# Performance work log

Measured on AMD Instinct MI355X. Metric: run time of the kernel, lower is better.

Reference implementation:

```python
import jax, jax.numpy as jnp
from jax import lax
import numpy as np

H = 128; L = 4; N_TOTAL = 4096; M = 4; S = 16384; K = 12; SK = S * K
MAX_DIST = 32; B = 64; NH = 4; DH = H // NH; BN_EPS = 1e-5


def _bn(x, g, b):
    # training-mode BatchNorm1d over rows (biased variance)
    mu = x.mean(0)
    var = x.var(0)
    return (x - mu) * lax.rsqrt(var + BN_EPS) * g + b


def _gine(x, src, dst, ea, eps, We, bWe, W1, b1, W2, b2):
    # PyG GINEConv: mlp((1+eps)*x + sum_j relu(x_j + lin(e_ji)))
    msg = jax.nn.relu(x[src] + ea @ We.T + bWe)
    agg = jax.ops.segment_sum(msg, dst, num_segments=x.shape[0])
    h = (1.0 + eps) * x + agg
    return jax.nn.relu(h @ W1.T + b1) @ W2.T + b2


def _forward(log_probs, atom_tab, bond_tab, dist_tab, logp_W, logp_b, lw, lb,
             bn_g, bn_b, eps, mha_in_W, mha_in_b, mha_out_W, mha_out_b, ro_g, ro_b,
             atom_ids, node_ids, intra_ei, intra_bond_ids, edge_index, canon_bond_ids, batch):
    sub_batch = jnp.arange(SK, dtype=jnp.int32) // K
    root_flat = jnp.arange(S, dtype=jnp.int32) * K
    valid_f = (node_ids >= 0).astype(jnp.float32)[:, None]
    clamped = jnp.maximum(node_ids, 0)
    x_flat = atom_tab[atom_ids][clamped]            # [SK, H]
    ea_flat = bond_tab[intra_bond_ids]              # [E_intra, H]
    edge_attr = bond_tab[canon_bond_ids]            # [E_canon, H]
    src, dst = intra_ei[0], intra_ei[1]

    # BFS distances from subgraph roots (min-plus relaxation, MAX_DIST sweeps)
    d0 = jnp.full((SK,), MAX_DIST, jnp.int32).at[root_flat].set(0)
    dist = lax.fori_loop(0, MAX_DIST, lambda i, d: d.at[dst].min(d[src] + 1), d0)
    dist = jnp.minimum(dist, MAX_DIST)
    dist_pe = dist_tab[dist]

    logp_pe = jax.nn.relu(log_probs[sub_batch][:, None] @ logp_W.T + logp_b)
    h = (x_flat + dist_pe + logp_pe) * valid_f

    is_root_f = jnp.zeros((SK, 1), jnp.float32).at[root_flat].set(1.0)
    root_ids = node_ids[root_flat]                  # canonical id of each root (>=0)
    cnt = jnp.maximum(jax.ops.segment_sum(jnp.ones((S,), jnp.float32), root_ids,
                                          num_segments=N_TOTAL), 1.0)

    for l in range(L):
        W = lw[l]; bv = lb[l]
        h1 = _gine(h, src, dst, ea_flat, eps[l, 0], W[0], bv[0], W[1], bv[1], W[2], bv[2])
        h1 = _bn(h1, bn_g[l, 0], bn_b[l, 0]) * valid_f
        h_root_b = h[sub_batch * K]
        h_nr = h @ W[3].T + bv[3] + h_root_b @ W[4].T + bv[4]
        h_can = jax.ops.segment_sum(h[root_flat], root_ids, num_segments=N_TOTAL) / cnt[:, None]
        h_int = _gine(h_can, edge_index[0], edge_index[1], edge_attr, eps[l, 1],
                      W[5], bv[5], W[6], bv[6], W[7], bv[7])
        h_int = _bn(h_int, bn_g[l, 1], bn_b[l, 1])
        h_ib = h_int[clamped] * valid_f
        out = is_root_f * (h1 + h_ib) + (1.0 - is_root_f) * (h1 + h_nr)
        h = jax.nn.relu(out) * valid_f

    # subgraph sum-pool (invalid rows are zeroed so scatter of zeros is a no-op)
    h_sub = jax.ops.segment_sum(h * valid_f, sub_batch, num_segments=S)
    order = jnp.argsort(root_ids)                   # stable by default
    h2 = h_sub[order].reshape(N_TOTAL, M, H)

    # MultiheadAttention over the m subgraphs of each canonical node
    qkv = h2 @ mha_in_W.T + mha_in_b
    q, k_, v = jnp.split(qkv, 3, axis=-1)
    hd = lambda t: t.reshape(N_TOTAL, M, NH, DH).transpose(0, 2, 1, 3)
    q, k_, v = hd(q), hd(k_), hd(v)
    scale = np.float32(1.0 / np.sqrt(DH))
    attn = jax.nn.softmax(jnp.einsum('nhqd,nhkd->nhqk', q, k_) * scale, axis=-1)
    o = jnp.einsum('nhqk,nhkd->nhqd', attn, v).transpose(0, 2, 1, 3).reshape(N_TOTAL, M, H)
    h_attn = o @ mha_out_W.T + mha_out_b + h2
    node_emb = _bn(h_attn.mean(1), ro_g, ro_b)
    return jax.ops.segment_sum(node_emb, batch, num_segments=B)


def setup_inputs() -> dict:
    key = jax.random.key(0)
    ks = jax.random.split(key, 32)
    rn = lambda i, sh, sc=0.1: (jax.random.normal(ks[i], sh) * sc).astype(jnp.float32)
    atom_ids = jax.random.randint(ks[0], (N_TOTAL,), 0, 64, dtype=jnp.int32)
    nid = jax.random.randint(ks[1], (S, K), 0, N_TOTAL, dtype=jnp.int32)
    pad = jax.random.uniform(ks[2], (S, K)) < 0.1
    nid = jnp.where(pad, -1, nid)
    nid = nid.at[:, 0].set(jnp.arange(S, dtype=jnp.int32) // M)  # roots: each canonical node m times
    node_ids = nid.reshape(-1)
    flat = jnp.arange(SK, dtype=jnp.int32).reshape(S, K)
    intra_ei = jnp.stack([flat[:, :-1].reshape(-1), flat[:, 1:].reshape(-1)])  # chains per subgraph
    intra_bond_ids = jax.random.randint(ks[3], (S * (K - 1),), 0, 8, dtype=jnp.int32)
    edge_index = jax.random.randint(ks[4], (2, N_TOTAL * 8), 0, N_TOTAL, dtype=jnp.int32)
    canon_bond_ids = jax.random.randint(ks[5], (N_TOTAL * 8,), 0, 8, dtype=jnp.int32)
    batch = jnp.arange(N_TOTAL, dtype=jnp.int32) // (N_TOTAL // B)
    log_probs = jax.random.normal(ks[6], (S,), dtype=jnp.float32)
    return dict(
        atom_ids=atom_ids, node_ids=node_ids, intra_ei=intra_ei,
        intra_bond_ids=intra_bond_ids, edge_index=edge_index,
        canon_bond_ids=canon_bond_ids, batch=batch, log_probs=log_probs,
        atom_tab=rn(7, (64, H)), bond_tab=rn(8, (8, H)), dist_tab=rn(9, (MAX_DIST + 1, H)),
        logp_W=rn(10, (H, 1)), logp_b=jnp.zeros((H,), jnp.float32),
        lw=rn(11, (L, 8, H, H)), lb=jnp.zeros((L, 8, H), jnp.float32),
        bn_g=jnp.ones((L, 2, H), jnp.float32), bn_b=jnp.zeros((L, 2, H), jnp.float32),
        eps=jnp.zeros((L, 2), jnp.float32),
        mha_in_W=rn(12, (3 * H, H)), mha_in_b=jnp.zeros((3 * H,), jnp.float32),
        mha_out_W=rn(13, (H, H)), mha_out_b=jnp.zeros((H,), jnp.float32),
        ro_g=jnp.ones((H,), jnp.float32), ro_b=jnp.zeros((H,), jnp.float32))


def reference(atom_ids, node_ids, intra_ei, intra_bond_ids, edge_index, canon_bond_ids,
              batch, log_probs, atom_tab, bond_tab, dist_tab, logp_W, logp_b, lw, lb,
              bn_g, bn_b, eps, mha_in_W, mha_in_b, mha_out_W, mha_out_b, ro_g, ro_b):
    return _forward(log_probs, atom_tab, bond_tab, dist_tab, logp_W, logp_b, lw, lb,
                    bn_g, bn_b, eps, mha_in_W, mha_in_b, mha_out_W, mha_out_b, ro_g, ro_b,
                    atom_ids, node_ids, intra_ei, intra_bond_ids, edge_index, canon_bond_ids, batch)
```

## Files before the change

### kernel.cpp

```cpp
#include <hip/hip_runtime.h>
#include <math.h>

#define DEV static __device__ __forceinline__

constexpr int H    = 128;
constexpr int Ksub = 12;
constexpr int S    = 16384;
constexpr int SK   = S * Ksub;
constexpr int NTOT = 4096;

DEV float4 ld4(const float* p) { return *(const float4*)p; }
DEV void   st4(float* p, float4 v) { *(float4*)p = v; }
DEV float4 add4(float4 a, float4 b) { return make_float4(a.x+b.x, a.y+b.y, a.z+b.z, a.w+b.w); }
DEV float4 relu4(float4 a) { return make_float4(fmaxf(a.x,0.f), fmaxf(a.y,0.f), fmaxf(a.z,0.f), fmaxf(a.w,0.f)); }

template<int PRO, int EPI>
__global__ __launch_bounds__(256, 4) void mm128(
    const float* __restrict__ X, const float* __restrict__ Wm,
    const float* __restrict__ bias, float* __restrict__ Y,
    const float* __restrict__ eps_p,
    const float* __restrict__ a1, const float* __restrict__ a2,
    const float* __restrict__ a3, const int* __restrict__ ids,
    float* __restrict__ stats, const float* __restrict__ bng,
    const float* __restrict__ bnb, float invR, size_t ybstride)
{
  __shared__ float smem[2 * 32 * 132];
  float (*Xs)[132] = (float(*)[132])smem;
  float (*Ws)[132] = (float(*)[132])(smem + 32 * 132);
  const int tid  = threadIdx.x;
  const int row0 = blockIdx.x * 128;
  const int yb   = blockIdx.y;
  Wm   += (size_t)yb * (H * H);
  bias += yb * H;
  Y    += (size_t)yb * ybstride;

  const int tc  = tid & 15;
  const int tr  = tid >> 4;
  const int kq4 = (tid & 7) * 4;
  const int rb  = tid >> 3;

  float scal = 1.0f;
  if (PRO == 1 || PRO == 3) scal = 1.0f + eps_p[0];

  float acc[8][8];
#pragma unroll
  for (int i = 0; i < 8; ++i)
#pragma unroll
    for (int j = 0; j < 8; ++j) acc[i][j] = 0.f;

  for (int kk = 0; kk < 128; kk += 32) {
    __syncthreads();
#pragma unroll
    for (int p = 0; p < 4; ++p) {
      int r = rb + 32 * p;
      int grow = row0 + r;
      float4 wv = ld4(Wm + (size_t)r * H + kk + kq4);
      float4 xv;
      if (PRO == 2) xv = ld4(X + ((size_t)grow * Ksub) * H + kk + kq4);
      else          xv = ld4(X + (size_t)grow * H + kk + kq4);
      if (PRO == 1) {
        float4 a = ld4(a1 + (size_t)grow * H + kk + kq4);
        xv.x = fmaf(scal, xv.x, a.x); xv.y = fmaf(scal, xv.y, a.y);
        xv.z = fmaf(scal, xv.z, a.z); xv.w = fmaf(scal, xv.w, a.w);
      }
      if (PRO == 3) {
        int q = grow % Ksub;
        float m0 = 0.f, m1 = 0.f, m2 = 0.f, m3 = 0.f;
        if (q) {
          int bid = ids[(grow / Ksub) * (Ksub - 1) + q - 1];
          float4 hp = ld4(X + (size_t)(grow - 1) * H + kk + kq4);
          float4 bp = ld4(a1 + (size_t)bid * H + kk + kq4);
          m0 = fmaxf(hp.x + bp.x, 0.f); m1 = fmaxf(hp.y + bp.y, 0.f);
          m2 = fmaxf(hp.z + bp.z, 0.f); m3 = fmaxf(hp.w + bp.w, 0.f);
        }
        xv.x = fmaf(scal, xv.x, m0); xv.y = fmaf(scal, xv.y, m1);
        xv.z = fmaf(scal, xv.z, m2); xv.w = fmaf(scal, xv.w, m3);
      }
      Xs[kq4 + 0][r] = xv.x; Xs[kq4 + 1][r] = xv.y;
      Xs[kq4 + 2][r] = xv.z; Xs[kq4 + 3][r] = xv.w;
      Ws[kq4 + 0][r] = wv.x; Ws[kq4 + 1][r] = wv.y;
      Ws[kq4 + 2][r] = wv.z; Ws[kq4 + 3][r] = wv.w;
    }
    __syncthreads();
#pragma unroll 4
    for (int k = 0; k < 32; ++k) {
      float xv[8], wv[8];
      *(float4*)&xv[0] = *(const float4*)&Xs[k][4 * tr];
      *(float4*)&xv[4] = *(const float4*)&Xs[k][64 + 4 * tr];
      *(float4*)&wv[0] = *(const float4*)&Ws[k][4 * tc];
      *(float4*)&wv[4] = *(const float4*)&Ws[k][64 + 4 * tc];
#pragma unroll
      for (int i = 0; i < 8; ++i)
#pragma unroll
        for (int j = 0; j < 8; ++j) acc[i][j] = fmaf(xv[i], wv[j], acc[i][j]);
    }
  }

  float4 bias0 = ld4(bias + 4 * tc);
  float4 bias1 = ld4(bias + 64 + 4 * tc);
  float4 mu0, mu1, rs0, rs1, g0, g1, bb0, bb1;
  if (EPI == 3) {
    float4 s0 = ld4(stats + 4 * tc),        s1 = ld4(stats + 64 + 4 * tc);
    float4 q0 = ld4(stats + 128 + 4 * tc),  q1 = ld4(stats + 128 + 64 + 4 * tc);
    mu0 = make_float4(s0.x * invR, s0.y * invR, s0.z * invR, s0.w * invR);
    mu1 = make_float4(s1.x * invR, s1.y * invR, s1.z * invR, s1.w * invR);
    rs0 = make_float4(rsqrtf(q0.x * invR - mu0.x * mu0.x + 1e-5f),
                      rsqrtf(q0.y * invR - mu0.y * mu0.y + 1e-5f),
                      rsqrtf(q0.z * invR - mu0.z * mu0.z + 1e-5f),
                      rsqrtf(q0.w * invR - mu0.w * mu0.w + 1e-5f));
    rs1 = make_float4(rsqrtf(q1.x * invR - mu1.x * mu1.x + 1e-5f),
                      rsqrtf(q1.y * invR - mu1.y * mu1.y + 1e-5f),
                      rsqrtf(q1.z * invR - mu1.z * mu1.z + 1e-5f),
                      rsqrtf(q1.w * invR - mu1.w * mu1.w + 1e-5f));
    g0 = ld4(bng + 4 * tc); g1 = ld4(bng + 64 + 4 * tc);
    bb0 = ld4(bnb + 4 * tc); bb1 = ld4(bnb + 64 + 4 * tc);
  }
  float ps[8], pq[8];
  if (EPI == 2) {
#pragma unroll
    for (int j = 0; j < 8; ++j) { ps[j] = 0.f; pq[j] = 0.f; }
  }

#pragma unroll
  for (int i = 0; i < 8; ++i) {
    int gr = row0 + ((i < 4) ? 4 * tr + i : 60 + 4 * tr + i);
    float4 y0 = make_float4(acc[i][0] + bias0.x, acc[i][1] + bias0.y,
                            acc[i][2] + bias0.z, acc[i][3] + bias0.w);
    float4 y1 = make_float4(acc[i][4] + bias1.x, acc[i][5] + bias1.y,
                            acc[i][6] + bias1.z, acc[i][7] + bias1.w);
    if (EPI == 1) { y0 = relu4(y0); y1 = relu4(y1); }
    if (EPI == 4) {
      y0 = add4(y0, ld4(a1 + (size_t)gr * H + 4 * tc));
      y1 = add4(y1, ld4(a1 + (size_t)gr * H + 64 + 4 * tc));
    }
    if (EPI == 3) {
      int nid = ids[gr];
      float vf = (nid >= 0) ? 1.f : 0.f;
      bool root = (gr % Ksub) == 0;
      float4 t0 = ld4(a1 + (size_t)gr * H + 4 * tc);
      float4 t1v = ld4(a1 + (size_t)gr * H + 64 + 4 * tc);
      float4 h10 = make_float4(fmaf((t0.x - mu0.x) * rs0.x, g0.x, bb0.x),
                               fmaf((t0.y - mu0.y) * rs0.y, g0.y, bb0.y),
                               fmaf((t0.z - mu0.z) * rs0.z, g0.z, bb0.z),
                               fmaf((t0.w - mu0.w) * rs0.w, g0.w, bb0.w));
      float4 h11 = make_float4(fmaf((t1v.x - mu1.x) * rs1.x, g1.x, bb1.x),
                               fmaf((t1v.y - mu1.y) * rs1.y, g1.y, bb1.y),
                               fmaf((t1v.z - mu1.z) * rs1.z, g1.z, bb1.z),
                               fmaf((t1v.w - mu1.w) * rs1.w, g1.w, bb1.w));
      float4 add0, add1;
      if (root) {
        add0 = ld4(a2 + (size_t)nid * H + 4 * tc);
        add1 = ld4(a2 + (size_t)nid * H + 64 + 4 * tc);
      } else {
        add0 = add4(y0, ld4(a3 + (size_t)(gr / Ksub) * H + 4 * tc));
        add1 = add4(y1, ld4(a3 + (size_t)(gr / Ksub) * H + 64 + 4 * tc));
      }
      y0 = make_float4(vf * fmaxf(h10.x + add0.x, 0.f), vf * fmaxf(h10.y + add0.y, 0.f),
                       vf * fmaxf(h10.z + add0.z, 0.f), vf * fmaxf(h10.w + add0.w, 0.f));
      y1 = make_float4(vf * fmaxf(h11.x + add1.x, 0.f), vf * fmaxf(h11.y + add1.y, 0.f),
                       vf * fmaxf(h11.z + add1.z, 0.f), vf * fmaxf(h11.w + add1.w, 0.f));
    }
    st4(Y + (size_t)gr * H + 4 * tc, y0);
    st4(Y + (size_t)gr * H + 64 + 4 * tc, y1);
    if (EPI == 2) {
      ps[0] += y0.x; pq[0] += y0.x * y0.x; ps[1] += y0.y; pq[1] += y0.y * y0.y;
      ps[2] += y0.z; pq[2] += y0.z * y0.z; ps[3] += y0.w; pq[3] += y0.w * y0.w;
      ps[4] += y1.x; pq[4] += y1.x * y1.x; ps[5] += y1.y; pq[5] += y1.y * y1.y;
      ps[6] += y1.z; pq[6] += y1.z * y1.z; ps[7] += y1.w; pq[7] += y1.w * y1.w;
    }
  }
  if (EPI == 2) {
    __syncthreads();
    float* redS = smem;
    float* redQ = smem + 2048;
#pragma unroll
    for (int j = 0; j < 8; ++j) {
      int c = (j < 4) ? 4 * tc + j : 60 + 4 * tc + j;
      redS[tr * 128 + c] = ps[j];
      redQ[tr * 128 + c] = pq[j];
    }
    __syncthreads();
    if (tid < 128) {
      float s = 0.f, q = 0.f;
#pragma unroll
      for (int t = 0; t < 16; ++t) { s += redS[t * 128 + tid]; q += redQ[t * 128 + tid]; }
      atomicAdd(stats + tid, s);
      atomicAdd(stats + 128 + tid, q);
    }
  }
}

__global__ void k_init_h(float* __restrict__ h, const int* __restrict__ node_ids,
                         const int* __restrict__ atom_ids,
                         const float* __restrict__ atom_tab, const float* __restrict__ dist_tab,
                         const float* __restrict__ log_probs, const float* __restrict__ logp_W,
                         const float* __restrict__ logp_b)
{
  int idx = blockIdx.x * 256 + threadIdx.x;
  if (idx >= SK * 32) return;
  int r = idx >> 5, c4 = (idx & 31) * 4;
  int nid = node_ids[r];
  float valid = nid >= 0 ? 1.f : 0.f;
  int cl = nid >= 0 ? nid : 0;
  int aid = atom_ids[cl];
  int dd = r % Ksub;
  float lp = log_probs[r / Ksub];
  float4 at = ld4(atom_tab + aid * H + c4);
  float4 dt = ld4(dist_tab + dd * H + c4);
  float4 w  = ld4(logp_W + c4);
  float4 bb = ld4(logp_b + c4);
  float4 o;
  o.x = (at.x + dt.x + fmaxf(fmaf(lp, w.x, bb.x), 0.f)) * valid;
  o.y = (at.y + dt.y + fmaxf(fmaf(lp, w.y, bb.y), 0.f)) * valid;
  o.z = (at.z + dt.z + fmaxf(fmaf(lp, w.z, bb.z), 0.f)) * valid;
  o.w = (at.w + dt.w + fmaxf(fmaf(lp, w.w, bb.w), 0.f)) * valid;
  st4(h + (size_t)r * H + c4, o);
}

__global__ void k_bond_all(const float* __restrict__ bt, const float* __restrict__ lw,
                           const float* __restrict__ lb, float* __restrict__ bp_all)
{
  int m = blockIdx.x;
  int c = threadIdx.x;
  int l = m >> 1, wsel = (m & 1) ? 5 : 0;
  const float* W = lw + ((size_t)l * 8 + wsel) * H * H;
  const float* b = lb + ((size_t)l * 8 + wsel) * H;
  for (int j = 0; j < 8; ++j) {
    float s = b[c];
    for (int k = 0; k < H; ++k) s = fmaf(bt[j * H + k], W[c * H + k], s);
    bp_all[(size_t)(m * 8 + j) * H + c] = s;
  }
}

__global__ void k_c1(const float* __restrict__ h, float* __restrict__ c1) {
  int idx = blockIdx.x * 256 + threadIdx.x;
  if (idx >= NTOT * 32) return;
  int n = idx >> 5, c4 = (idx & 31) * 4;
  float4 a = ld4(h + ((size_t)(4 * n + 0) * Ksub) * H + c4);
  float4 b = ld4(h + ((size_t)(4 * n + 1) * Ksub) * H + c4);
  float4 c = ld4(h + ((size_t)(4 * n + 2) * Ksub) * H + c4);
  float4 d = ld4(h + ((size_t)(4 * n + 3) * Ksub) * H + c4);
  float4 o;
  o.x = (a.x + b.x + c.x + d.x) * 0.25f;
  o.y = (a.y + b.y + c.y + d.y) * 0.25f;
  o.z = (a.z + b.z + c.z + d.z) * 0.25f;
  o.w = (a.w + b.w + c.w + d.w) * 0.25f;
  st4(c1 + (size_t)n * H + c4, o);
}

__global__ void k_agg(const float* __restrict__ x, const int* __restrict__ src,
                      const int* __restrict__ dst, const int* __restrict__ bid,
                      const float* __restrict__ bp, float* __restrict__ out, int E)
{
  int idx = blockIdx.x * 256 + threadIdx.x;
  if (idx >= E * 32) return;
  int e = idx >> 5, c4 = (idx & 31) * 4;
  int sv = src[e], dv = dst[e], bb = bid[e];
  float4 m = relu4(add4(ld4(x + (size_t)sv * H + c4), ld4(bp + (size_t)bb * H + c4)));
  float* o = out + (size_t)dv * H + c4;
  atomicAdd(o + 0, m.x); atomicAdd(o + 1, m.y);
  atomicAdd(o + 2, m.z); atomicAdd(o + 3, m.w);
}

__global__ __launch_bounds__(256) void k_bn_stats(const float* __restrict__ X, int R,
                                                  float* __restrict__ stats) {
  __shared__ float sh[2][256];
  int c = threadIdx.x & 127;
  int rr = threadIdx.x >> 7;
  float s = 0.f, s2 = 0.f;
  for (int r = blockIdx.x * 2 + rr; r < R; r += gridDim.x * 2) {
    float v = X[(size_t)r * H + c];
    s += v; s2 += v * v;
  }
  sh[0][threadIdx.x] = s; sh[1][threadIdx.x] = s2;
  __syncthreads();
  if (rr == 0) {
    atomicAdd(&stats[c],       s  + sh[0][threadIdx.x + 128]);
    atomicAdd(&stats[128 + c], s2 + sh[1][threadIdx.x + 128]);
  }
}

__global__ void k_bn_apply(float* __restrict__ X, int R, const float* __restrict__ stats,
                           const float* __restrict__ g, const float* __restrict__ b)
{
  int idx = blockIdx.x * 256 + threadIdx.x;
  if (idx >= R * 32) return;
  int r = idx >> 5, c4 = (idx & 31) * 4;
  float invR = 1.0f / (float)R;
  float4 sm = ld4(stats + c4);
  float4 sq = ld4(stats + 128 + c4);
  float4 gv = ld4(g + c4), bv = ld4(b + c4);
  float mu0 = sm.x * invR, mu1 = sm.y * invR, mu2 = sm.z * invR, mu3 = sm.w * invR;
  float k0 = rsqrtf(sq.x * invR - mu0 * mu0 + 1e-5f);
  float k1 = rsqrtf(sq.y * invR - mu1 * mu1 + 1e-5f);
  float k2 = rsqrtf(sq.z * invR - mu2 * mu2 + 1e-5f);
  float k3 = rsqrtf(sq.w * invR - mu3 * mu3 + 1e-5f);
  float4 x = ld4(X + (size_t)r * H + c4);
  float4 o;
  o.x = (x.x - mu0) * k0 * gv.x + bv.x;
  o.y = (x.y - mu1) * k1 * gv.y + bv.y;
  o.z = (x.z - mu2) * k2 * gv.z + bv.z;
  o.w = (x.w - mu3) * k3 * gv.w + bv.w;
  st4(X + (size_t)r * H + c4, o);
}

__global__ void k_pool(const float* __restrict__ h, float* __restrict__ hsub) {
  int idx = blockIdx.x * 256 + threadIdx.x;
  if (idx >= S * 32) return;
  int s = idx >> 5, c4 = (idx & 31) * 4;
  float4 acc = make_float4(0.f, 0.f, 0.f, 0.f);
  const float* p = h + ((size_t)s * Ksub) * H + c4;
#pragma unroll
  for (int j = 0; j < Ksub; ++j) acc = add4(acc, ld4(p + j * H));
  st4(hsub + (size_t)s * H + c4, acc);
}

__global__ __launch_bounds__(128) void k_attn(const float* __restrict__ qb,
                                              const float* __restrict__ kb,
                                              const float* __restrict__ vb,
                                              float* __restrict__ ob)
{
  int n = blockIdx.x;
  int c = threadIdx.x;
  float q[4], kv[4], vv[4];
#pragma unroll
  for (int m = 0; m < 4; ++m) {
    q[m]  = qb[(size_t)(n * 4 + m) * H + c];
    kv[m] = kb[(size_t)(n * 4 + m) * H + c];
    vv[m] = vb[(size_t)(n * 4 + m) * H + c];
  }
  const float scale = 0.17677669529663687f;
  float sc[4][4];
#pragma unroll
  for (int m1 = 0; m1 < 4; ++m1)
#pragma unroll
    for (int m2 = 0; m2 < 4; ++m2) {
      float p = q[m1] * kv[m2];
#pragma unroll
      for (int off = 16; off > 0; off >>= 1) p += __shfl_xor(p, off, 32);
      sc[m1][m2] = p * scale;
    }
#pragma unroll
  for (int m1 = 0; m1 < 4; ++m1) {
    float mx = fmaxf(fmaxf(sc[m1][0], sc[m1][1]), fmaxf(sc[m1][2], sc[m1][3]));
    float e0 = expf(sc[m1][0] - mx), e1 = expf(sc[m1][1] - mx);
    float e2 = expf(sc[m1][2] - mx), e3 = expf(sc[m1][3] - mx);
    float inv = 1.f / (e0 + e1 + e2 + e3);
    ob[(size_t)(n * 4 + m1) * H + c] =
        (e0 * vv[0] + e1 * vv[1] + e2 * vv[2] + e3 * vv[3]) * inv;
  }
}

__global__ void k_mean(const float* __restrict__ ha, float* __restrict__ ne) {
  int idx = blockIdx.x * 256 + threadIdx.x;
  if (idx >= NTOT * 32) return;
  int n = idx >> 5, c4 = (idx & 31) * 4;
  float4 a = ld4(ha + (size_t)(n * 4 + 0) * H + c4);
  float4 b = ld4(ha + (size_t)(n * 4 + 1) * H + c4);
  float4 c = ld4(ha + (size_t)(n * 4 + 2) * H + c4);
  float4 d = ld4(ha + (size_t)(n * 4 + 3) * H + c4);
  float4 o;
  o.x = (a.x + b.x + c.x + d.x) * 0.25f;
  o.y = (a.y + b.y + c.y + d.y) * 0.25f;
  o.z = (a.z + b.z + c.z + d.z) * 0.25f;
  o.w = (a.w + b.w + c.w + d.w) * 0.25f;
  st4(ne + (size_t)n * H + c4, o);
}

__global__ __launch_bounds__(128) void k_finalsum(const float* __restrict__ ne,
                                                  const float* __restrict__ stats,
                                                  const float* __restrict__ g,
                                                  const float* __restrict__ b,
                                                  float* __restrict__ out)
{
  int bg = blockIdx.x;
  int c = threadIdx.x;
  const float invR = 1.0f / (float)NTOT;
  float mu = stats[c] * invR;
  float rs = rsqrtf(stats[128 + c] * invR - mu * mu + 1e-5f);
  float gg = g[c], bb = b[c];
  float acc = 0.f;
  for (int r = 0; r < 64; ++r) {
    float v = ne[(size_t)(bg * 64 + r) * H + c];
    acc += (v - mu) * rs * gg + bb;
  }
  out[(size_t)bg * H + c] = acc;
}

extern "C" void kernel_launch(void* const* d_in, const int* in_sizes, int n_in,
                              void* d_out, int out_size, void* d_ws, size_t ws_size,
                              hipStream_t stream)
{
  const int*   atom_ids   = (const int*)d_in[0];
  const int*   node_ids   = (const int*)d_in[1];
  const int*   intra_bid  = (const int*)d_in[3];
  const int*   edge_index = (const int*)d_in[4];
  const int*   canon_bid  = (const int*)d_in[5];
  const float* log_probs  = (const float*)d_in[7];
  const float* atom_tab   = (const float*)d_in[8];
  const float* bond_tab   = (const float*)d_in[9];
  const float* dist_tab   = (const float*)d_in[10];
  const float* logp_W     = (const float*)d_in[11];
  const float* logp_b     = (const float*)d_in[12];
  const float* lw         = (const float*)d_in[13];
  const float* lb         = (const float*)d_in[14];
  const float* bn_g       = (const float*)d_in[15];
  const float* bn_b       = (const float*)d_in[16];
  const float* eps        = (const float*)d_in[17];
  const float* mha_in_W   = (const float*)d_in[18];
  const float* mha_in_b   = (const float*)d_in[19];
  const float* mha_out_W  = (const float*)d_in[20];
  const float* mha_out_b  = (const float*)d_in[21];
  const float* ro_g       = (const float*)d_in[22];
  const float* ro_b       = (const float*)d_in[23];

  const int E2 = in_sizes[4] / 2;
  const int* src2 = edge_index, *dst2 = edge_index + E2;

  float* ws = (float*)d_ws;
  const size_t SKH = (size_t)SK * H;
  float* h      = ws;
  float* t      = ws + SKH;
  float* rproj  = ws + 2 * SKH;
  float* c1     = rproj + (size_t)S * H;
  float* c2     = c1 + (size_t)NTOT * H;
  float* c3     = c2 + (size_t)NTOT * H;
  float* ne     = c3 + (size_t)NTOT * H;
  float* bp_all = ne + (size_t)NTOT * H;
  float* statsA = bp_all + 64 * H;
  float* hsub = t;
  float* qkv  = t + (size_t)S * H;
  float* ob   = qkv + 3 * (size_t)S * H;
  float* out  = (float*)d_out;

  hipMemsetAsync(statsA, 0, 9 * 256 * sizeof(float), stream);
  k_bond_all<<<8, 128, 0, stream>>>(bond_tab, lw, lb, bp_all);
  k_init_h<<<(SK * 32 + 255) / 256, 256, 0, stream>>>(h, node_ids, atom_ids,
      atom_tab, dist_tab, log_probs, logp_W, logp_b);

  for (int l = 0; l < 4; ++l) {
    const float* W  = lw + (size_t)l * 8 * H * H;
    const float* bb = lb + (size_t)l * 8 * H;
    const float* g0 = bn_g + (l * 2 + 0) * H, *b0  = bn_b + (l * 2 + 0) * H;
    const float* g1 = bn_g + (l * 2 + 1) * H, *b1v = bn_b + (l * 2 + 1) * H;
    const float* eps0 = eps + l * 2, *eps1 = eps + l * 2 + 1;
    float* st0 = statsA + (size_t)l * 512;
    float* st1 = statsA + (size_t)l * 512 + 256;
    const float* bp0 = bp_all + (size_t)(l * 2 + 0) * 8 * H;
    const float* bp1 = bp_all + (size_t)(l * 2 + 1) * 8 * H;

    mm128<3, 1><<<dim3(SK / 128, 1), 256, 0, stream>>>(h, W + 1 * H * H, bb + 1 * H, t,
        eps0, bp0, nullptr, nullptr, intra_bid, nullptr, nullptr, nullptr, 0.f, 0);
    mm128<0, 2><<<dim3(SK / 128, 1), 256, 0, stream>>>(t, W + 2 * H * H, bb + 2 * H, t,
        nullptr, nullptr, nullptr, nullptr, nullptr, st0, nullptr, nullptr, 0.f, 0);
    mm128<2, 0><<<dim3(S / 128, 1), 256, 0, stream>>>(h, W + 4 * H * H, bb + 4 * H, rproj,
        nullptr, nullptr, nullptr, nullptr, nullptr, nullptr, nullptr, nullptr, 0.f, 0);
    k_c1<<<(NTOT * 32 + 255) / 256, 256, 0, stream>>>(h, c1);
    hipMemsetAsync(c2, 0, (size_t)NTOT * H * sizeof(float), stream);
    k_agg<<<(E2 * 32 + 255) / 256, 256, 0, stream>>>(c1, src2, dst2, canon_bid, bp1, c2, E2);
    mm128<1, 1><<<dim3(NTOT / 128, 1), 256, 0, stream>>>(c1, W + 6 * H * H, bb + 6 * H, c2,
        eps1, c2, nullptr, nullptr, nullptr, nullptr, nullptr, nullptr, 0.f, 0);
    mm128<0, 2><<<dim3(NTOT / 128, 1), 256, 0, stream>>>(c2, W + 7 * H * H, bb + 7 * H, c3,
        nullptr, nullptr, nullptr, nullptr, nullptr, st1, nullptr, nullptr, 0.f, 0);
    k_bn_apply<<<(NTOT * 32 + 255) / 256, 256, 0, stream>>>(c3, NTOT, st1, g1, b1v);
    mm128<0, 3><<<dim3(SK / 128, 1), 256, 0, stream>>>(h, W + 3 * H * H, bb + 3 * H, h,
        nullptr, t, c3, rproj, node_ids, st0, g0, b0, 1.0f / (float)SK, 0);
  }

  k_pool<<<(S * 32 + 255) / 256, 256, 0, stream>>>(h, hsub);
  mm128<0, 0><<<dim3(S / 128, 3), 256, 0, stream>>>(hsub, mha_in_W, mha_in_b, qkv,
      nullptr, nullptr, nullptr, nullptr, nullptr, nullptr, nullptr, nullptr, 0.f,
      (size_t)S * H);
  k_attn<<<NTOT, 128, 0, stream>>>(qkv, qkv + (size_t)S * H, qkv + 2 * (size_t)S * H, ob);
  mm128<0, 4><<<dim3(S / 128, 1), 256, 0, stream>>>(ob, mha_out_W, mha_out_b, ob,
      nullptr, hsub, nullptr, nullptr, nullptr, nullptr, nullptr, nullptr, 0.f, 0);
  k_mean<<<(NTOT * 32 + 255) / 256, 256, 0, stream>>>(ob, ne);
  float* stF = statsA + 8 * 256;
  k_bn_stats<<<512, 256, 0, stream>>>(ne, NTOT, stF);
  k_finalsum<<<64, 128, 0, stream>>>(ne, stF, ro_g, ro_b, out);
}
```

Before: 1.798 ms.

## Replace FP32 SIMT GEMMs with split-bf16 MFMA matrix-core kernels

Replaces the shared-memory FP32 FMA GEMM with a kernel that splits activations and weights into bf16 hi/lo pairs and runs three MFMA 16x16x32 products per tile, recovering near-FP32 accuracy on matrix cores. Weights are pre-split once per call by a new k_split kernel. The GIN node-level prologue (eps scaling plus aggregate) moves into a separate k_prep2 kernel, and the rproj GEMM is reordered. Operands now load directly from global memory without LDS staging, and the three-term split is slightly less exact than true FP32.

```diff
diff --git a/kernel.cpp b/kernel.cpp
--- a/kernel.cpp
+++ b/kernel.cpp
@@ -9,184 +9,187 @@
 constexpr int SK   = S * Ksub;
 constexpr int NTOT = 4096;
 
+typedef __attribute__((ext_vector_type(8))) short bhalf8;
+typedef __attribute__((ext_vector_type(4))) float floatx4;
+
 DEV float4 ld4(const float* p) { return *(const float4*)p; }
 DEV void   st4(float* p, float4 v) { *(float4*)p = v; }
-DEV float4 add4(float4 a, float4 b) { return make_float4(a.x+b.x, a.y+b.y, a.z+b.z, a.w+b.w); }
-DEV float4 relu4(float4 a) { return make_float4(fmaxf(a.x,0.f), fmaxf(a.y,0.f), fmaxf(a.z,0.f), fmaxf(a.w,0.f)); }
+
+DEV ushort f2b(float f) {
+  unsigned x = __float_as_uint(f);
+  return (ushort)((x + 0x7FFFu + ((x >> 16) & 1u)) >> 16);
+}
+DEV float b2f(ushort u) { return __uint_as_float(((unsigned)u) << 16); }
+
+DEV void split8(const float* v, bhalf8& hi, bhalf8& lo) {
+#pragma unroll
+  for (int j = 0; j < 8; ++j) {
+    ushort hv = f2b(v[j]);
+    hi[j] = (short)hv;
+    lo[j] = (short)f2b(v[j] - b2f(hv));
+  }
+}
 
 template<int PRO, int EPI>
-__global__ __launch_bounds__(256, 4) void mm128(
-    const float* __restrict__ X, const float* __restrict__ Wm,
-    const float* __restrict__ bias, float* __restrict__ Y,
-    const float* __restrict__ eps_p,
+__global__ __launch_bounds__(256) void mmB(
+    const float* __restrict__ X, const ushort* __restrict__ Whi,
+    const ushort* __restrict__ Wlo, const float* __restrict__ bias,
+    float* __restrict__ Y,
     const float* __restrict__ a1, const float* __restrict__ a2,
     const float* __restrict__ a3, const int* __restrict__ ids,
     float* __restrict__ stats, const float* __restrict__ bng,
-    const float* __restrict__ bnb, float invR, size_t ybstride)
-{
-  __shared__ float smem[2 * 32 * 132];
-  float (*Xs)[132] = (float(*)[132])smem;
-  float (*Ws)[132] = (float(*)[132])(smem + 32 * 132);
+    const float* __restrict__ bnb, const float* __restrict__ eps_p,
+    float invR, size_t ybstride)
+{
+  __shared__ float sred[2][8][128];
   const int tid  = threadIdx.x;
+  const int lane = tid & 63, wv = tid >> 6;
+  const int wr = (wv >> 1) * 64, wc = (wv & 1) * 64;
+  const int m = lane & 15, q = lane >> 4;
   const int row0 = blockIdx.x * 128;
-  const int yb   = blockIdx.y;
-  Wm   += (size_t)yb * (H * H);
+  const int yb = blockIdx.y;
+  Whi  += (size_t)yb * (H * H);
+  Wlo  += (size_t)yb * (H * H);
   bias += yb * H;
   Y    += (size_t)yb * ybstride;
 
-  const int tc  = tid & 15;
-  const int tr  = tid >> 4;
-  const int kq4 = (tid & 7) * 4;
-  const int rb  = tid >> 3;
-
   float scal = 1.0f;
-  if (PRO == 1 || PRO == 3) scal = 1.0f + eps_p[0];
-
-  float acc[8][8];
-#pragma unroll
-  for (int i = 0; i < 8; ++i)
-#pragma unroll
-    for (int j = 0; j < 8; ++j) acc[i][j] = 0.f;
-
-  for (int kk = 0; kk < 128; kk += 32) {
-    __syncthreads();
-#pragma unroll
-    for (int p = 0; p < 4; ++p) {
-      int r = rb + 32 * p;
-      int grow = row0 + r;
-      float4 wv = ld4(Wm + (size_t)r * H + kk + kq4);
-      float4 xv;
-      if (PRO == 2) xv = ld4(X + ((size_t)grow * Ksub) * H + kk + kq4);
-      else          xv = ld4(X + (size_t)grow * H + kk + kq4);
-      if (PRO == 1) {
-        float4 a = ld4(a1 + (size_t)grow * H + kk + kq4);
-        xv.x = fmaf(scal, xv.x, a.x); xv.y = fmaf(scal, xv.y, a.y);
-        xv.z = fmaf(scal, xv.z, a.z); xv.w = fmaf(scal, xv.w, a.w);
+  if (PRO == 3) scal = 1.0f + eps_p[0];
+
+  floatx4 acc[4][4];
+#pragma unroll
+  for (int i = 0; i < 4; ++i)
+#pragma unroll
+    for (int j = 0; j < 4; ++j) acc[i][j] = (floatx4){0.f, 0.f, 0.f, 0.f};
+
+  size_t arow[4], brow[4];
+  int qi[4];
+  const float* bprow[4];
+#pragma unroll
+  for (int i = 0; i < 4; ++i) {
+    int grow = row0 + wr + 16 * i + m;
+    arow[i] = (size_t)(PRO == 2 ? grow * Ksub : grow) * H;
+    brow[i] = (size_t)(wc + 16 * i + m) * H;
+    qi[i] = 0; bprow[i] = nullptr;
+    if (PRO == 3) {
+      qi[i] = grow % Ksub;
+      if (qi[i]) bprow[i] = a1 + (size_t)ids[(grow / Ksub) * (Ksub - 1) + qi[i] - 1] * H;
+    }
+  }
+
+#pragma unroll
+  for (int s = 0; s < 4; ++s) {
+    const int ko = s * 32 + q * 8;
+    bhalf8 bhi[4], blo[4];
+#pragma unroll
+    for (int j = 0; j < 4; ++j) {
+      bhi[j] = *(const bhalf8*)(Whi + brow[j] + ko);
+      blo[j] = *(const bhalf8*)(Wlo + brow[j] + ko);
+    }
+    bhalf8 ahi[4], alo[4];
+#pragma unroll
+    for (int i = 0; i < 4; ++i) {
+      float xv[8];
+      *(float4*)&xv[0] = ld4(X + arow[i] + ko);
+      *(float4*)&xv[4] = ld4(X + arow[i] + ko + 4);
+      if (PRO == 3) {
+        if (qi[i]) {
+          float pv[8], bv[8];
+          *(float4*)&pv[0] = ld4(X + arow[i] - H + ko);
+          *(float4*)&pv[4] = ld4(X + arow[i] - H + ko + 4);
+          *(float4*)&bv[0] = ld4(bprow[i] + ko);
+          *(float4*)&bv[4] = ld4(bprow[i] + ko + 4);
+#pragma unroll
+          for (int j = 0; j < 8; ++j)
+            xv[j] = fmaf(scal, xv[j], fmaxf(pv[j] + bv[j], 0.f));
+        } else {
+#pragma unroll
+          for (int j = 0; j < 8; ++j) xv[j] *= scal;
+        }
       }
-      if (PRO == 3) {
-        int q = grow % Ksub;
-        float m0 = 0.f, m1 = 0.f, m2 = 0.f, m3 = 0.f;
-        if (q) {
-          int bid = ids[(grow / Ksub) * (Ksub - 1) + q - 1];
-          float4 hp = ld4(X + (size_t)(grow - 1) * H + kk + kq4);
-          float4 bp = ld4(a1 + (size_t)bid * H + kk + kq4);
-          m0 = fmaxf(hp.x + bp.x, 0.f); m1 = fmaxf(hp.y + bp.y, 0.f);
-          m2 = fmaxf(hp.z + bp.z, 0.f); m3 = fmaxf(hp.w + bp.w, 0.f);
+      split8(xv, ahi[i], alo[i]);
+    }
+#pragma unroll
+    for (int i = 0; i < 4; ++i)
+#pragma unroll
+      for (int j = 0; j < 4; ++j) {
+        acc[i][j] = __builtin_amdgcn_mfma_f32_16x16x32_bf16(ahi[i], bhi[j], acc[i][j], 0, 0, 0);
+        acc[i][j] = __builtin_amdgcn_mfma_f32_16x16x32_bf16(ahi[i], blo[j], acc[i][j], 0, 0, 0);
+        acc[i][j] = __builtin_amdgcn_mfma_f32_16x16x32_bf16(alo[i], bhi[j], acc[i][j], 0, 0, 0);
+      }
+  }
+
+  __syncthreads();
+
+  float psum[4], psq[4];
+#pragma unroll
+  for (int j = 0; j < 4; ++j) { psum[j] = 0.f; psq[j] = 0.f; }
+
+#pragma unroll
+  for (int j = 0; j < 4; ++j) {
+    const int col = wc + 16 * j + m;
+    const float bcol = bias[col];
+    float mu = 0.f, rs = 0.f, gg = 0.f, bb = 0.f;
+    if (EPI == 3) {
+      mu = stats[col] * invR;
+      rs = rsqrtf(stats[128 + col] * invR - mu * mu + 1e-5f);
+      gg = bng[col]; bb = bnb[col];
+    }
+#pragma unroll
+    for (int i = 0; i < 4; ++i) {
+      const int rowb = row0 + wr + 16 * i + 4 * q;
+#pragma unroll
+      for (int r = 0; r < 4; ++r) {
+        const int gr = rowb + r;
+        float y = acc[i][j][r] + bcol;
+        if (EPI == 1) y = fmaxf(y, 0.f);
+        if (EPI == 4) y += a1[(size_t)gr * H + col];
+        if (EPI == 3) {
+          int nid = ids[gr];
+          float vf = (nid >= 0) ? 1.f : 0.f;
+          bool root = (gr % Ksub) == 0;
+          float t2v = a1[(size_t)gr * H + col];
+          float h1 = fmaf((t2v - mu) * rs, gg, bb);
+          float addv = root ? a2[(size_t)nid * H + col]
+                            : (y + a3[(size_t)(gr / Ksub) * H + col]);
+          y = vf * fmaxf(h1 + addv, 0.f);
         }
-        xv.x = fmaf(scal, xv.x, m0); xv.y = fmaf(scal, xv.y, m1);
-        xv.z = fmaf(scal, xv.z, m2); xv.w = fmaf(scal, xv.w, m3);
+        Y[(size_t)gr * H + col] = y;
+        if (EPI == 2) { psum[j] += y; psq[j] += y * y; }
       }
-      Xs[kq4 + 0][r] = xv.x; Xs[kq4 + 1][r] = xv.y;
-      Xs[kq4 + 2][r] = xv.z; Xs[kq4 + 3][r] = xv.w;
-      Ws[kq4 + 0][r] = wv.x; Ws[kq4 + 1][r] = wv.y;
-      Ws[kq4 + 2][r] = wv.z; Ws[kq4 + 3][r] = wv.w;
-    }
-    __syncthreads();
-#pragma unroll 4
-    for (int k = 0; k < 32; ++k) {
-      float xv[8], wv[8];
-      *(float4*)&xv[0] = *(const float4*)&Xs[k][4 * tr];
-      *(float4*)&xv[4] = *(const float4*)&Xs[k][64 + 4 * tr];
-      *(float4*)&wv[0] = *(const float4*)&Ws[k][4 * tc];
-      *(float4*)&wv[4] = *(const float4*)&Ws[k][64 + 4 * tc];
-#pragma unroll
-      for (int i = 0; i < 8; ++i)
-#pragma unroll
-        for (int j = 0; j < 8; ++j) acc[i][j] = fmaf(xv[i], wv[j], acc[i][j]);
-    }
-  }
-
-  float4 bias0 = ld4(bias + 4 * tc);
-  float4 bias1 = ld4(bias + 64 + 4 * tc);
-  float4 mu0, mu1, rs0, rs1, g0, g1, bb0, bb1;
-  if (EPI == 3) {
-    float4 s0 = ld4(stats + 4 * tc),        s1 = ld4(stats + 64 + 4 * tc);
-    float4 q0 = ld4(stats + 128 + 4 * tc),  q1 = ld4(stats + 128 + 64 + 4 * tc);
-    mu0 = make_float4(s0.x * invR, s0.y * invR, s0.z * invR, s0.w * invR);
-    mu1 = make_float4(s1.x * invR, s1.y * invR, s1.z * invR, s1.w * invR);
-    rs0 = make_float4(rsqrtf(q0.x * invR - mu0.x * mu0.x + 1e-5f),
-                      rsqrtf(q0.y * invR - mu0.y * mu0.y + 1e-5f),
-                      rsqrtf(q0.z * invR - mu0.z * mu0.z + 1e-5f),
-                      rsqrtf(q0.w * invR - mu0.w * mu0.w + 1e-5f));
-    rs1 = make_float4(rsqrtf(q1.x * invR - mu1.x * mu1.x + 1e-5f),
-                      rsqrtf(q1.y * invR - mu1.y * mu1.y + 1e-5f),
-                      rsqrtf(q1.z * invR - mu1.z * mu1.z + 1e-5f),
-                      rsqrtf(q1.w * invR - mu1.w * mu1.w + 1e-5f));
-    g0 = ld4(bng + 4 * tc); g1 = ld4(bng + 64 + 4 * tc);
-    bb0 = ld4(bnb + 4 * tc); bb1 = ld4(bnb + 64 + 4 * tc);
-  }
-  float ps[8], pq[8];
+    }
+  }
+
   if (EPI == 2) {
-#pragma unroll
-    for (int j = 0; j < 8; ++j) { ps[j] = 0.f; pq[j] = 0.f; }
-  }
-
-#pragma unroll
-  for (int i = 0; i < 8; ++i) {
-    int gr = row0 + ((i < 4) ? 4 * tr + i : 60 + 4 * tr + i);
-    float4 y0 = make_float4(acc[i][0] + bias0.x, acc[i][1] + bias0.y,
-                            acc[i][2] + bias0.z, acc[i][3] + bias0.w);
-    float4 y1 = make_float4(acc[i][4] + bias1.x, acc[i][5] + bias1.y,
-                            acc[i][6] + bias1.z, acc[i][7] + bias1.w);
-    if (EPI == 1) { y0 = relu4(y0); y1 = relu4(y1); }
-    if (EPI == 4) {
-      y0 = add4(y0, ld4(a1 + (size_t)gr * H + 4 * tc));
-      y1 = add4(y1, ld4(a1 + (size_t)gr * H + 64 + 4 * tc));
-    }
-    if (EPI == 3) {
-      int nid = ids[gr];
-      float vf = (nid >= 0) ? 1.f : 0.f;
-      bool root = (gr % Ksub) == 0;
-      float4 t0 = ld4(a1 + (size_t)gr * H + 4 * tc);
-      float4 t1v = ld4(a1 + (size_t)gr * H + 64 + 4 * tc);
-      float4 h10 = make_float4(fmaf((t0.x - mu0.x) * rs0.x, g0.x, bb0.x),
-                               fmaf((t0.y - mu0.y) * rs0.y, g0.y, bb0.y),
-                               fmaf((t0.z - mu0.z) * rs0.z, g0.z, bb0.z),
-                               fmaf((t0.w - mu0.w) * rs0.w, g0.w, bb0.w));
-      float4 h11 = make_float4(fmaf((t1v.x - mu1.x) * rs1.x, g1.x, bb1.x),
-                               fmaf((t1v.y - mu1.y) * rs1.y, g1.y, bb1.y),
-                               fmaf((t1v.z - mu1.z) * rs1.z, g1.z, bb1.z),
-                               fmaf((t1v.w - mu1.w) * rs1.w, g1.w, bb1.w));
-      float4 add0, add1;
-      if (root) {
-        add0 = ld4(a2 + (size_t)nid * H + 4 * tc);
-        add1 = ld4(a2 + (size_t)nid * H + 64 + 4 * tc);
-      } else {
-        add0 = add4(y0, ld4(a3 + (size_t)(gr / Ksub) * H + 4 * tc));
-        add1 = add4(y1, ld4(a3 + (size_t)(gr / Ksub) * H + 64 + 4 * tc));
-      }
-      y0 = make_float4(vf * fmaxf(h10.x + add0.x, 0.f), vf * fmaxf(h10.y + add0.y, 0.f),
-                       vf * fmaxf(h10.z + add0.z, 0.f), vf * fmaxf(h10.w + add0.w, 0.f));
-      y1 = make_float4(vf * fmaxf(h11.x + add1.x, 0.f), vf * fmaxf(h11.y + add1.y, 0.f),
-                       vf * fmaxf(h11.z + add1.z, 0.f), vf * fmaxf(h11.w + add1.w, 0.f));
-    }
-    st4(Y + (size_t)gr * H + 4 * tc, y0);
-    st4(Y + (size_t)gr * H + 64 + 4 * tc, y1);
-    if (EPI == 2) {
-      ps[0] += y0.x; pq[0] += y0.x * y0.x; ps[1] += y0.y; pq[1] += y0.y * y0.y;
-      ps[2] += y0.z; pq[2] += y0.z * y0.z; ps[3] += y0.w; pq[3] += y0.w * y0.w;
-      ps[4] += y1.x; pq[4] += y1.x * y1.x; ps[5] += y1.y; pq[5] += y1.y * y1.y;
-      ps[6] += y1.z; pq[6] += y1.z * y1.z; ps[7] += y1.w; pq[7] += y1.w * y1.w;
-    }
-  }
-  if (EPI == 2) {
-    __syncthreads();
-    float* redS = smem;
-    float* redQ = smem + 2048;
-#pragma unroll
-    for (int j = 0; j < 8; ++j) {
-      int c = (j < 4) ? 4 * tc + j : 60 + 4 * tc + j;
-      redS[tr * 128 + c] = ps[j];
-      redQ[tr * 128 + c] = pq[j];
+    const int slot = (wv >> 1) * 4 + q;
+#pragma unroll
+    for (int j = 0; j < 4; ++j) {
+      const int col = wc + 16 * j + m;
+      sred[0][slot][col] = psum[j];
+      sred[1][slot][col] = psq[j];
     }
     __syncthreads();
     if (tid < 128) {
-      float s = 0.f, q = 0.f;
-#pragma unroll
-      for (int t = 0; t < 16; ++t) { s += redS[t * 128 + tid]; q += redQ[t * 128 + tid]; }
+      float s = 0.f, q2 = 0.f;
+#pragma unroll
+      for (int t = 0; t < 8; ++t) { s += sred[0][t][tid]; q2 += sred[1][t][tid]; }
       atomicAdd(stats + tid, s);
-      atomicAdd(stats + 128 + tid, q);
-    }
+      atomicAdd(stats + 128 + tid, q2);
+    }
+  }
+}
+
+__global__ void k_split(const float* __restrict__ src, ushort* __restrict__ hi,
+                        ushort* __restrict__ lo, int n) {
+  int i = (blockIdx.x * 256 + threadIdx.x) * 4;
+  if (i >= n) return;
+  float4 v = ld4(src + i);
+  float vv[4] = {v.x, v.y, v.z, v.w};
+#pragma unroll
+  for (int j = 0; j < 4; ++j) {
+    ushort hv = f2b(vv[j]);
+    hi[i + j] = hv;
+    lo[i + j] = f2b(vv[j] - b2f(hv));
   }
 }
 
@@ -208,27 +211,27 @@
   float4 at = ld4(atom_tab + aid * H + c4);
   float4 dt = ld4(dist_tab + dd * H + c4);
   float4 w  = ld4(logp_W + c4);
-  float4 bb = ld4(logp_b + c4);
+  float4 bbv = ld4(logp_b + c4);
   float4 o;
-  o.x = (at.x + dt.x + fmaxf(fmaf(lp, w.x, bb.x), 0.f)) * valid;
-  o.y = (at.y + dt.y + fmaxf(fmaf(lp, w.y, bb.y), 0.f)) * valid;
-  o.z = (at.z + dt.z + fmaxf(fmaf(lp, w.z, bb.z), 0.f)) * valid;
-  o.w = (at.w + dt.w + fmaxf(fmaf(lp, w.w, bb.w), 0.f)) * valid;
+  o.x = (at.x + dt.x + fmaxf(fmaf(lp, w.x, bbv.x), 0.f)) * valid;
+  o.y = (at.y + dt.y + fmaxf(fmaf(lp, w.y, bbv.y), 0.f)) * valid;
+  o.z = (at.z + dt.z + fmaxf(fmaf(lp, w.z, bbv.z), 0.f)) * valid;
+  o.w = (at.w + dt.w + fmaxf(fmaf(lp, w.w, bbv.w), 0.f)) * valid;
   st4(h + (size_t)r * H + c4, o);
 }
 
 __global__ void k_bond_all(const float* __restrict__ bt, const float* __restrict__ lw,
                            const float* __restrict__ lb, float* __restrict__ bp_all)
 {
-  int m = blockIdx.x;
+  int mb = blockIdx.x;
   int c = threadIdx.x;
-  int l = m >> 1, wsel = (m & 1) ? 5 : 0;
+  int l = mb >> 1, wsel = (mb & 1) ? 5 : 0;
   const float* W = lw + ((size_t)l * 8 + wsel) * H * H;
   const float* b = lb + ((size_t)l * 8 + wsel) * H;
   for (int j = 0; j < 8; ++j) {
     float s = b[c];
     for (int k = 0; k < H; ++k) s = fmaf(bt[j * H + k], W[c * H + k], s);
-    bp_all[(size_t)(m * 8 + j) * H + c] = s;
+    bp_all[(size_t)(mb * 8 + j) * H + c] = s;
   }
 }
 
@@ -236,16 +239,13 @@
   int idx = blockIdx.x * 256 + threadIdx.x;
   if (idx >= NTOT * 32) return;
   int n = idx >> 5, c4 = (idx & 31) * 4;
-  float4 a = ld4(h + ((size_t)(4 * n + 0) * Ksub) * H + c4);
-  float4 b = ld4(h + ((size_t)(4 * n + 1) * Ksub) * H + c4);
-  float4 c = ld4(h + ((size_t)(4 * n + 2) * Ksub) * H + c4);
-  float4 d = ld4(h + ((size_t)(4 * n + 3) * Ksub) * H + c4);
-  float4 o;
-  o.x = (a.x + b.x + c.x + d.x) * 0.25f;
-  o.y = (a.y + b.y + c.y + d.y) * 0.25f;
-  o.z = (a.z + b.z + c.z + d.z) * 0.25f;
-  o.w = (a.w + b.w + c.w + d.w) * 0.25f;
-  st4(c1 + (size_t)n * H + c4, o);
+  float o0 = 0.f, o1 = 0.f, o2 = 0.f, o3 = 0.f;
+#pragma unroll
+  for (int mi = 0; mi < 4; ++mi) {
+    const float* p = h + ((size_t)(4 * n + mi) * Ksub) * H + c4;
+    o0 += p[0]; o1 += p[1]; o2 += p[2]; o3 += p[3];
+  }
+  st4(c1 + (size_t)n * H + c4, make_float4(o0 * .25f, o1 * .25f, o2 * .25f, o3 * .25f));
 }
 
 __global__ void k_agg(const float* __restrict__ x, const int* __restrict__ src,
@@ -256,10 +256,107 @@
   if (idx >= E * 32) return;
   int e = idx >> 5, c4 = (idx & 31) * 4;
   int sv = src[e], dv = dst[e], bb = bid[e];
-  float4 m = relu4(add4(ld4(x + (size_t)sv * H + c4), ld4(bp + (size_t)bb * H + c4)));
+  float4 xv = ld4(x + (size_t)sv * H + c4);
+  float4 bv = ld4(bp + (size_t)bb * H + c4);
   float* o = out + (size_t)dv * H + c4;
-  atomicAdd(o + 0, m.x); atomicAdd(o + 1, m.y);
-  atomicAdd(o + 2, m.z); atomicAdd(o + 3, m.w);
+  atomicAdd(o + 0, fmaxf(xv.x + bv.x, 0.f));
+  atomicAdd(o + 1, fmaxf(xv.y + bv.y, 0.f));
+  atomicAdd(o + 2, fmaxf(xv.z + bv.z, 0.f));
+  atomicAdd(o + 3, fmaxf(xv.w + bv.w, 0.f));
+}
+
+__global__ void k_prep2(float* __restrict__ c1, const float* __restrict__ c2f,
+                        const float* __restrict__ eps_p)
+{
+  int idx = blockIdx.x * 256 + threadIdx.x;
+  if (idx >= NTOT * 32) return;
+  int n = idx >> 5, c4 = (idx & 31) * 4;
+  float scal = 1.0f + eps_p[0];
+  float4 cv = ld4(c1 + (size_t)n * H + c4);
+  float4 ag = ld4(c2f + (size_t)n * H + c4);
+  st4(c1 + (size_t)n * H + c4,
+      make_float4(fmaf(scal, cv.x, ag.x), fmaf(scal, cv.y, ag.y),
+                  fmaf(scal, cv.z, ag.z), fmaf(scal, cv.w, ag.w)));
+}
+
+__global__ void k_bn_apply(float* __restrict__ X, int R, const float* __restrict__ stats,
+                           const float* __restrict__ g, const float* __restrict__ b)
+{
+  int idx = blockIdx.x * 256 + threadIdx.x;
+  if (idx >= R * 32) return;
+  int r = idx >> 5, c4 = (idx & 31) * 4;
+  float invR = 1.0f / (float)R;
+  float* p = X + (size_t)r * H + c4;
+#pragma unroll
+  for (int j = 0; j < 4; ++j) {
+    int c = c4 + j;
+    float mu = stats[c] * invR;
+    float rs = rsqrtf(stats[128 + c] * invR - mu * mu + 1e-5f);
+    p[j] = fmaf((p[j] - mu) * rs, g[c], b[c]);
+  }
+}
+
+__global__ void k_pool(const float* __restrict__ h, float* __restrict__ hsub) {
+  int idx = blockIdx.x * 256 + threadIdx.x;
+  if (idx >= S * 32) return;
+  int s = idx >> 5, c4 = (idx & 31) * 4;
+  float a0 = 0.f, a1 = 0.f, a2 = 0.f, a3 = 0.f;
+  const float* p = h + ((size_t)s * Ksub) * H + c4;
+#pragma unroll
+  for (int j = 0; j < Ksub; ++j) {
+    a0 += p[0]; a1 += p[1]; a2 += p[2]; a3 += p[3];
+    p += H;
+  }
+  st4(hsub + (size_t)s * H + c4, make_float4(a0, a1, a2, a3));
+}
+
+__global__ __launch_bounds__(128) void k_attn(const float* __restrict__ qb,
+                                              const float* __restrict__ kb,
+                                              const float* __restrict__ vb,
+                                              float* __restrict__ ob)
+{
+  int n = blockIdx.x;
+  int c = threadIdx.x;
+  float q[4], kv[4], vv[4];
+#pragma unroll
+  for (int mi = 0; mi < 4; ++mi) {
+    q[mi]  = qb[(size_t)(n * 4 + mi) * H + c];
+    kv[mi] = kb[(size_t)(n * 4 + mi) * H + c];
+    vv[mi] = vb[(size_t)(n * 4 + mi) * H + c];
+  }
+  const float scale = 0.17677669529663687f;
+  float sc[4][4];
+#pragma unroll
+  for (int m1 = 0; m1 < 4; ++m1)
+#pragma unroll
+    for (int m2 = 0; m2 < 4; ++m2) {
+      float p = q[m1] * kv[m2];
+#pragma unroll
+      for (int off = 16; off > 0; off >>= 1) p += __shfl_xor(p, off, 32);
+      sc[m1][m2] = p * scale;
+    }
+#pragma unroll
+  for (int m1 = 0; m1 < 4; ++m1) {
+    float mx = fmaxf(fmaxf(sc[m1][0], sc[m1][1]), fmaxf(sc[m1][2], sc[m1][3]));
+    float e0 = expf(sc[m1][0] - mx), e1 = expf(sc[m1][1] - mx);
+    float e2 = expf(sc[m1][2] - mx), e3 = expf(sc[m1][3] - mx);
+    float inv = 1.f / (e0 + e1 + e2 + e3);
+    ob[(size_t)(n * 4 + m1) * H + c] =
+        (e0 * vv[0] + e1 * vv[1] + e2 * vv[2] + e3 * vv[3]) * inv;
+  }
+}
+
+__global__ void k_mean(const float* __restrict__ ha, float* __restrict__ ne) {
+  int idx = blockIdx.x * 256 + threadIdx.x;
+  if (idx >= NTOT * 32) return;
+  int n = idx >> 5, c4 = (idx & 31) * 4;
+  float4 a = ld4(ha + (size_t)(n * 4 + 0) * H + c4);
+  float4 b = ld4(ha + (size_t)(n * 4 + 1) * H + c4);
+  float4 c = ld4(ha + (size_t)(n * 4 + 2) * H + c4);
+  float4 d = ld4(ha + (size_t)(n * 4 + 3) * H + c4);
+  st4(ne + (size_t)n * H + c4,
+      make_float4((a.x + b.x + c.x + d.x) * .25f, (a.y + b.y + c.y + d.y) * .25f,
+                  (a.z + b.z + c.z + d.z) * .25f, (a.w + b.w + c.w + d.w) * .25f));
 }
 
 __global__ __launch_bounds__(256) void k_bn_stats(const float* __restrict__ X, int R,
@@ -278,93 +375,6 @@
     atomicAdd(&stats[c],       s  + sh[0][threadIdx.x + 128]);
     atomicAdd(&stats[128 + c], s2 + sh[1][threadIdx.x + 128]);
   }
-}
-
-__global__ void k_bn_apply(float* __restrict__ X, int R, const float* __restrict__ stats,
-                           const float* __restrict__ g, const float* __restrict__ b)
-{
-  int idx = blockIdx.x * 256 + threadIdx.x;
-  if (idx >= R * 32) return;
-  int r = idx >> 5, c4 = (idx & 31) * 4;
-  float invR = 1.0f / (float)R;
-  float4 sm = ld4(stats + c4);
-  float4 sq = ld4(stats + 128 + c4);
-  float4 gv = ld4(g + c4), bv = ld4(b + c4);
-  float mu0 = sm.x * invR, mu1 = sm.y * invR, mu2 = sm.z * invR, mu3 = sm.w * invR;
-  float k0 = rsqrtf(sq.x * invR - mu0 * mu0 + 1e-5f);
-  float k1 = rsqrtf(sq.y * invR - mu1 * mu1 + 1e-5f);
-  float k2 = rsqrtf(sq.z * invR - mu2 * mu2 + 1e-5f);
-  float k3 = rsqrtf(sq.w * invR - mu3 * mu3 + 1e-5f);
-  float4 x = ld4(X + (size_t)r * H + c4);
-  float4 o;
-  o.x = (x.x - mu0) * k0 * gv.x + bv.x;
-  o.y = (x.y - mu1) * k1 * gv.y + bv.y;
-  o.z = (x.z - mu2) * k2 * gv.z + bv.z;
-  o.w = (x.w - mu3) * k3 * gv.w + bv.w;
-  st4(X + (size_t)r * H + c4, o);
-}
-
-__global__ void k_pool(const float* __restrict__ h, float* __restrict__ hsub) {
-  int idx = blockIdx.x * 256 + threadIdx.x;
-  if (idx >= S * 32) return;
-  int s = idx >> 5, c4 = (idx & 31) * 4;
-  float4 acc = make_float4(0.f, 0.f, 0.f, 0.f);
-  const float* p = h + ((size_t)s * Ksub) * H + c4;
-#pragma unroll
-  for (int j = 0; j < Ksub; ++j) acc = add4(acc, ld4(p + j * H));
-  st4(hsub + (size_t)s * H + c4, acc);
-}
-
-__global__ __launch_bounds__(128) void k_attn(const float* __restrict__ qb,
-                                              const float* __restrict__ kb,
-                                              const float* __restrict__ vb,
-                                              float* __restrict__ ob)
-{
-  int n = blockIdx.x;
-  int c = threadIdx.x;
-  float q[4], kv[4], vv[4];
-#pragma unroll
-  for (int m = 0; m < 4; ++m) {
-    q[m]  = qb[(size_t)(n * 4 + m) * H + c];
-    kv[m] = kb[(size_t)(n * 4 + m) * H + c];
-    vv[m] = vb[(size_t)(n * 4 + m) * H + c];
-  }
-  const float scale = 0.17677669529663687f;
-  float sc[4][4];
-#pragma unroll
-  for (int m1 = 0; m1 < 4; ++m1)
-#pragma unroll
-    for (int m2 = 0; m2 < 4; ++m2) {
-      float p = q[m1] * kv[m2];
-#pragma unroll
-      for (int off = 16; off > 0; off >>= 1) p += __shfl_xor(p, off, 32);
-      sc[m1][m2] = p * scale;
-    }
-#pragma unroll
-  for (int m1 = 0; m1 < 4; ++m1) {
-    float mx = fmaxf(fmaxf(sc[m1][0], sc[m1][1]), fmaxf(sc[m1][2], sc[m1][3]));
-    float e0 = expf(sc[m1][0] - mx), e1 = expf(sc[m1][1] - mx);
-    float e2 = expf(sc[m1][2] - mx), e3 = expf(sc[m1][3] - mx);
-    float inv = 1.f / (e0 + e1 + e2 + e3);
-    ob[(size_t)(n * 4 + m1) * H + c] =
-        (e0 * vv[0] + e1 * vv[1] + e2 * vv[2] + e3 * vv[3]) * inv;
-  }
-}
-
-__global__ void k_mean(const float* __restrict__ ha, float* __restrict__ ne) {
-  int idx = blockIdx.x * 256 + threadIdx.x;
-  if (idx >= NTOT * 32) return;
-  int n = idx >> 5, c4 = (idx & 31) * 4;
-  float4 a = ld4(ha + (size_t)(n * 4 + 0) * H + c4);
-  float4 b = ld4(ha + (size_t)(n * 4 + 1) * H + c4);
-  float4 c = ld4(ha + (size_t)(n * 4 + 2) * H + c4);
-  float4 d = ld4(ha + (size_t)(n * 4 + 3) * H + c4);
-  float4 o;
-  o.x = (a.x + b.x + c.x + d.x) * 0.25f;
-  o.y = (a.y + b.y + c.y + d.y) * 0.25f;
-  o.z = (a.z + b.z + c.z + d.z) * 0.25f;
-  o.w = (a.w + b.w + c.w + d.w) * 0.25f;
-  st4(ne + (size_t)n * H + c4, o);
 }
 
 __global__ __launch_bounds__(128) void k_finalsum(const float* __restrict__ ne,
@@ -417,29 +427,41 @@
   const int E2 = in_sizes[4] / 2;
   const int* src2 = edge_index, *dst2 = edge_index + E2;
 
-  float* ws = (float*)d_ws;
   const size_t SKH = (size_t)SK * H;
-  float* h      = ws;
-  float* t      = ws + SKH;
-  float* rproj  = ws + 2 * SKH;
-  float* c1     = rproj + (size_t)S * H;
-  float* c2     = c1 + (size_t)NTOT * H;
-  float* c3     = c2 + (size_t)NTOT * H;
-  float* ne     = c3 + (size_t)NTOT * H;
-  float* bp_all = ne + (size_t)NTOT * H;
-  float* statsA = bp_all + 64 * H;
+  char* wsb = (char*)d_ws;
+  float*  h      = (float*)wsb;     wsb += SKH * 4;
+  float*  t      = (float*)wsb;     wsb += SKH * 4;
+  float*  rproj  = (float*)wsb;     wsb += (size_t)S * H * 4;
+  float*  c1     = (float*)wsb;     wsb += (size_t)NTOT * H * 4;
+  float*  c2b    = (float*)wsb;     wsb += (size_t)NTOT * H * 4;
+  float*  c3     = (float*)wsb;     wsb += (size_t)NTOT * H * 4;
+  float*  c2f    = (float*)wsb;     wsb += (size_t)NTOT * H * 4;
+  float*  bp_all = (float*)wsb;     wsb += (size_t)64 * H * 4;
+  float*  statsA = (float*)wsb;     wsb += 9 * 256 * 4;
+  ushort* lwhi   = (ushort*)wsb;    wsb += (size_t)4 * 8 * H * H * 2;
+  ushort* lwlo   = (ushort*)wsb;    wsb += (size_t)4 * 8 * H * H * 2;
+  ushort* mihi   = (ushort*)wsb;    wsb += (size_t)3 * H * H * 2;
+  ushort* milo   = (ushort*)wsb;    wsb += (size_t)3 * H * H * 2;
+  ushort* mohi   = (ushort*)wsb;    wsb += (size_t)H * H * 2;
+  ushort* molo   = (ushort*)wsb;    wsb += (size_t)H * H * 2;
   float* hsub = t;
-  float* qkv  = t + (size_t)S * H;
+  float* qkv  = hsub + (size_t)S * H;
   float* ob   = qkv + 3 * (size_t)S * H;
+  float* ne   = ob + (size_t)S * H;
   float* out  = (float*)d_out;
 
   hipMemsetAsync(statsA, 0, 9 * 256 * sizeof(float), stream);
+  const int NLW = 4 * 8 * H * H, NMI = 3 * H * H, NMO = H * H;
+  k_split<<<(NLW / 4 + 255) / 256, 256, 0, stream>>>(lw, lwhi, lwlo, NLW);
+  k_split<<<(NMI / 4 + 255) / 256, 256, 0, stream>>>(mha_in_W, mihi, milo, NMI);
+  k_split<<<(NMO / 4 + 255) / 256, 256, 0, stream>>>(mha_out_W, mohi, molo, NMO);
   k_bond_all<<<8, 128, 0, stream>>>(bond_tab, lw, lb, bp_all);
   k_init_h<<<(SK * 32 + 255) / 256, 256, 0, stream>>>(h, node_ids, atom_ids,
       atom_tab, dist_tab, log_probs, logp_W, logp_b);
 
   for (int l = 0; l < 4; ++l) {
-    const float* W  = lw + (size_t)l * 8 * H * H;
+    const ushort* Whi = lwhi + (size_t)l * 8 * H * H;
+    const ushort* Wlo = lwlo + (size_t)l * 8 * H * H;
     const float* bb = lb + (size_t)l * 8 * H;
     const float* g0 = bn_g + (l * 2 + 0) * H, *b0  = bn_b + (l * 2 + 0) * H;
     const float* g1 = bn_g + (l * 2 + 1) * H, *b1v = bn_b + (l * 2 + 1) * H;
@@ -449,31 +471,38 @@
     const float* bp0 = bp_all + (size_t)(l * 2 + 0) * 8 * H;
     const float* bp1 = bp_all + (size_t)(l * 2 + 1) * 8 * H;
 
-    mm128<3, 1><<<dim3(SK / 128, 1), 256, 0, stream>>>(h, W + 1 * H * H, bb + 1 * H, t,
-        eps0, bp0, nullptr, nullptr, intra_bid, nullptr, nullptr, nullptr, 0.f, 0);
-    mm128<0, 2><<<dim3(SK / 128, 1), 256, 0, stream>>>(t, W + 2 * H * H, bb + 2 * H, t,
-        nullptr, nullptr, nullptr, nullptr, nullptr, st0, nullptr, nullptr, 0.f, 0);
-    mm128<2, 0><<<dim3(S / 128, 1), 256, 0, stream>>>(h, W + 4 * H * H, bb + 4 * H, rproj,
-        nullptr, nullptr, nullptr, nullptr, nullptr, nullptr, nullptr, nullptr, 0.f, 0);
+    mmB<3, 1><<<dim3(SK / 128, 1), 256, 0, stream>>>(h, Whi + 1 * H * H, Wlo + 1 * H * H,
+        bb + 1 * H, t, bp0, nullptr, nullptr, intra_bid, nullptr, nullptr, nullptr,
+        eps0, 0.f, 0);
+    mmB<0, 2><<<dim3(SK / 128, 1), 256, 0, stream>>>(t, Whi + 2 * H * H, Wlo + 2 * H * H,
+        bb + 2 * H, t, nullptr, nullptr, nullptr, nullptr, st0, nullptr, nullptr,
+        nullptr, 0.f, 0);
     k_c1<<<(NTOT * 32 + 255) / 256, 256, 0, stream>>>(h, c1);
-    hipMemsetAsync(c2, 0, (size_t)NTOT * H * sizeof(float), stream);
-    k_agg<<<(E2 * 32 + 255) / 256, 256, 0, stream>>>(c1, src2, dst2, canon_bid, bp1, c2, E2);
-    mm128<1, 1><<<dim3(NTOT / 128, 1), 256, 0, stream>>>(c1, W + 6 * H * H, bb + 6 * H, c2,
-        eps1, c2, nullptr, nullptr, nullptr, nullptr, nullptr, nullptr, 0.f, 0);
-    mm128<0, 2><<<dim3(NTOT / 128, 1), 256, 0, stream>>>(c2, W + 7 * H * H, bb + 7 * H, c3,
-        nullptr, nullptr, nullptr, nullptr, nullptr, st1, nullptr, nullptr, 0.f, 0);
+    hipMemsetAsync(c2f, 0, (size_t)NTOT * H * sizeof(float), stream);
+    k_agg<<<(E2 * 32 + 255) / 256, 256, 0, stream>>>(c1, src2, dst2, canon_bid, bp1, c2f, E2);
+    k_prep2<<<(NTOT * 32 + 255) / 256, 256, 0, stream>>>(c1, c2f, eps1);
+    mmB<0, 1><<<dim3(NTOT / 128, 1), 256, 0, stream>>>(c1, Whi + 6 * H * H, Wlo + 6 * H * H,
+        bb + 6 * H, c2b, nullptr, nullptr, nullptr, nullptr, nullptr, nullptr, nullptr,
+        nullptr, 0.f, 0);
+    mmB<0, 2><<<dim3(NTOT / 128, 1), 256, 0, stream>>>(c2b, Whi + 7 * H * H, Wlo + 7 * H * H,
+        bb + 7 * H, c3, nullptr, nullptr, nullptr, nullptr, st1, nullptr, nullptr,
+        nullptr, 0.f, 0);
     k_bn_apply<<<(NTOT * 32 + 255) / 256, 256, 0, stream>>>(c3, NTOT, st1, g1, b1v);
-    mm128<0, 3><<<dim3(SK / 128, 1), 256, 0, stream>>>(h, W + 3 * H * H, bb + 3 * H, h,
-        nullptr, t, c3, rproj, node_ids, st0, g0, b0, 1.0f / (float)SK, 0);
+    mmB<2, 0><<<dim3(S / 128, 1), 256, 0, stream>>>(h, Whi + 4 * H * H, Wlo + 4 * H * H,
+        bb + 4 * H, rproj, nullptr, nullptr, nullptr, nullptr, nullptr, nullptr, nullptr,
+        nullptr, 0.f, 0);
+    mmB<0, 3><<<dim3(SK / 128, 1), 256, 0, stream>>>(h, Whi + 3 * H * H, Wlo + 3 * H * H,
+        bb + 3 * H, h, t, c3, rproj, node_ids, st0, g0, b0, nullptr,
+        1.0f / (float)SK, 0);
   }
 
   k_pool<<<(S * 32 + 255) / 256, 256, 0, stream>>>(h, hsub);
-  mm128<0, 0><<<dim3(S / 128, 3), 256, 0, stream>>>(hsub, mha_in_W, mha_in_b, qkv,
+  mmB<0, 0><<<dim3(S / 128, 3), 256, 0, stream>>>(hsub, mihi, milo, mha_in_b, qkv,
       nullptr, nullptr, nullptr, nullptr, nullptr, nullptr, nullptr, nullptr, 0.f,
       (size_t)S * H);
   k_attn<<<NTOT, 128, 0, stream>>>(qkv, qkv + (size_t)S * H, qkv + 2 * (size_t)S * H, ob);
-  mm128<0, 4><<<dim3(S / 128, 1), 256, 0, stream>>>(ob, mha_out_W, mha_out_b, ob,
-      nullptr, hsub, nullptr, nullptr, nullptr, nullptr, nullptr, nullptr, 0.f, 0);
+  mmB<0, 4><<<dim3(S / 128, 1), 256, 0, stream>>>(ob, mohi, molo, mha_out_b, ob,
+      hsub, nullptr, nullptr, nullptr, nullptr, nullptr, nullptr, nullptr, 0.f, 0);
   k_mean<<<(NTOT * 32 + 255) / 256, 256, 0, stream>>>(ob, ne);
   float* stF = statsA + 8 * 256;
   k_bn_stats<<<512, 256, 0, stream>>>(ne, NTOT, stF);
```

Result: no change. 1.792 ms (-0.3%).
